# Optimization experiments

Measured on AMD Instinct MI355X. Metric: run time of the kernel, lower is better.

The kernel has to match this reference:

```python
import jax, jax.numpy as jnp
import numpy as np

V, D, H, NB, K = 50257, 768, 128, 4, 4  # vocab, d_model, d_hidden, n_blocks, conv kernel
B, L = 2, 1024


def setup_inputs() -> dict:
    key = jax.random.key(0)
    ks = jax.random.split(key, 8)
    s = 0.02
    return {
        "x": jax.random.randint(ks[0], (B, L), 0, V),
        "embed": jax.random.normal(ks[1], (V, D), jnp.float32) * s,   # tied embedding/head
        "conv_w": jax.random.normal(ks[2], (NB, D, K), jnp.float32) * s,  # depthwise causal conv
        "conv_b": jnp.zeros((NB, D), jnp.float32),
        "W_delta": jax.random.normal(ks[3], (NB, D, H), jnp.float32) * s,
        "b_delta": jnp.zeros((NB, H), jnp.float32),
        "W_in": jax.random.normal(ks[4], (NB, D, H), jnp.float32) * s,
        "W_out": jax.random.normal(ks[5], (NB, H, D), jnp.float32) * s,
        "log_A": jnp.log(jnp.tile(jnp.arange(1, H + 1, dtype=jnp.float32), (NB, 1))),
        "gamma": jnp.ones((D,), jnp.float32),
        "beta": jnp.zeros((D,), jnp.float32),
    }


def _mamba_block(x, cw, cb, Wd, bd, Win, Wout, logA):
    # x: [B,L,D]; cw: [D,K] depthwise causal conv; SSM state size H (shared per example)
    Bsz, Ln, _ = x.shape
    Kk = cw.shape[-1]
    xp = jnp.pad(x, ((0, 0), (Kk - 1, 0), (0, 0)))  # left-pad for causality
    xc = sum(xp[:, j:j + Ln, :] * cw[:, j] for j in range(Kk)) + cb  # [B,L,D]
    u = jax.nn.silu(xc)
    delta = jax.nn.softplus(jnp.einsum('bld,dh->blh', u, Wd) + bd)   # [B,L,H]
    Bu = jnp.einsum('bld,dh->blh', u, Win)                            # [B,L,H]
    A = -jnp.exp(logA)                                                # [H], negative
    decay = jnp.exp(delta * A)   # [B,L,H]
    inc = delta * Bu             # [B,L,H]

    def step(h, t):
        d, z = t
        h = d * h + z
        return h, h

    h0 = jnp.zeros((Bsz, decay.shape[-1]), x.dtype)
    _, hs = jax.lax.scan(step, h0, (decay.transpose(1, 0, 2), inc.transpose(1, 0, 2)))
    hs = hs.transpose(1, 0, 2)                                        # [B,L,H]
    y = jnp.einsum('blh,hd->bld', hs, Wout)
    return x + y  # residual


def reference(x, embed, conv_w, conv_b, W_delta, b_delta, W_in, W_out, log_A, gamma, beta):
    h = embed[x]  # [B,L,D]
    for i in range(conv_w.shape[0]):
        h = _mamba_block(h, conv_w[i], conv_b[i], W_delta[i], b_delta[i],
                         W_in[i], W_out[i], log_A[i])
    mu = jnp.mean(h, -1, keepdims=True)
    var = jnp.var(h, -1, keepdims=True)
    hn = (h - mu) * jax.lax.rsqrt(var + 1e-5) * gamma + beta  # LayerNorm
    return jnp.einsum('bld,vd->blv', hn, embed)  # tied-weight head -> [B,L,V]
```

## Files before the change

kernel.cpp:

```cpp
#include <hip/hip_runtime.h>

#define VSZ   50257
#define VPAD  50304
#define D_    768
#define H_    128
#define BL_   2048
#define LSEQ  1024

typedef __bf16 bf16x8 __attribute__((ext_vector_type(8)));
typedef float  f32x4  __attribute__((ext_vector_type(4)));

__device__ __forceinline__ unsigned short f32_to_bf16(float f) {
  unsigned int u = __float_as_uint(f);
  u += 0x7fffu + ((u >> 16) & 1u);
  return (unsigned short)(u >> 16);
}

__device__ __forceinline__ void gload_lds16(const void* g, void* l) {
  __builtin_amdgcn_global_load_lds((const __attribute__((address_space(1))) void*)g,
                                   (__attribute__((address_space(3))) void*)l,
                                   16, 0, 0);
}

__global__ __launch_bounds__(256) void convert_embed(const float* __restrict__ embed,
                                                     unsigned short* __restrict__ Eb) {
  int idx = blockIdx.x * 256 + threadIdx.x;
  int row = idx / 192;
  ushort4 o;
  if (row < VSZ) {
    float4 f = ((const float4*)embed)[idx];
    o.x = f32_to_bf16(f.x); o.y = f32_to_bf16(f.y);
    o.z = f32_to_bf16(f.z); o.w = f32_to_bf16(f.w);
  } else {
    o = make_ushort4(0, 0, 0, 0);
  }
  ((ushort4*)Eb)[idx] = o;
}

__global__ __launch_bounds__(256) void gather_embed(const int* __restrict__ x,
                                                    const float* __restrict__ embed,
                                                    float* __restrict__ h) {
  int idx = blockIdx.x * 256 + threadIdx.x;
  int m = idx / 192, d4 = idx - m * 192;
  int tok = x[m];
  ((float4*)h)[idx] = ((const float4*)embed)[(size_t)tok * 192 + d4];
}

__global__ __launch_bounds__(256) void conv_silu(const float* __restrict__ h,
                                                 const float* __restrict__ cw,
                                                 const float* __restrict__ cb,
                                                 float* __restrict__ u) {
  int idx = blockIdx.x * 256 + threadIdx.x;
  int m = idx / 192, d4 = idx - m * 192;
  int b = m >> 10, l = m & 1023;
  const float4* cw4 = (const float4*)cw;
  float4 w0 = cw4[d4 * 4 + 0], w1 = cw4[d4 * 4 + 1];
  float4 w2 = cw4[d4 * 4 + 2], w3 = cw4[d4 * 4 + 3];
  float4 acc = ((const float4*)cb)[d4];
  #pragma unroll
  for (int j = 0; j < 4; ++j) {
    int lj = l + j - 3;
    if (lj >= 0) {
      float4 xv = ((const float4*)h)[(size_t)((b << 10) + lj) * 192 + d4];
      acc.x += xv.x * (&w0.x)[j];
      acc.y += xv.y * (&w1.x)[j];
      acc.z += xv.z * (&w2.x)[j];
      acc.w += xv.w * (&w3.x)[j];
    }
  }
  acc.x = acc.x / (1.f + expf(-acc.x));
  acc.y = acc.y / (1.f + expf(-acc.y));
  acc.z = acc.z / (1.f + expf(-acc.z));
  acc.w = acc.w / (1.f + expf(-acc.w));
  ((float4*)u)[idx] = acc;
}

__global__ __launch_bounds__(256) void gemm_dbu(const float* __restrict__ u,
                                                const float* __restrict__ Wd,
                                                const float* __restrict__ Wi,
                                                float* __restrict__ pre) {
  __shared__ float Au[16 * 33];
  int m0 = blockIdx.x * 16;
  int sel = blockIdx.y;
  const float* W = sel ? Wi : Wd;
  int tid = threadIdx.x;
  int tm = tid & 7, tn = tid >> 3;
  float acc[2][4] = {};
  for (int k0 = 0; k0 < 768; k0 += 32) {
    __syncthreads();
    {
      int e = tid;        int mr = e >> 5, k = e & 31;
      Au[mr * 33 + k] = u[(size_t)(m0 + mr) * 768 + k0 + k];
      e = tid + 256;      mr = e >> 5;     k = e & 31;
      Au[mr * 33 + k] = u[(size_t)(m0 + mr) * 768 + k0 + k];
    }
    __syncthreads();
    #pragma unroll 8
    for (int k = 0; k < 32; ++k) {
      float4 w = *(const float4*)&W[(size_t)(k0 + k) * 128 + tn * 4];
      float a0 = Au[(tm * 2 + 0) * 33 + k];
      float a1 = Au[(tm * 2 + 1) * 33 + k];
      acc[0][0] += a0 * w.x; acc[0][1] += a0 * w.y; acc[0][2] += a0 * w.z; acc[0][3] += a0 * w.w;
      acc[1][0] += a1 * w.x; acc[1][1] += a1 * w.y; acc[1][2] += a1 * w.z; acc[1][3] += a1 * w.w;
    }
  }
  #pragma unroll
  for (int mi = 0; mi < 2; ++mi) {
    float4 o = make_float4(acc[mi][0], acc[mi][1], acc[mi][2], acc[mi][3]);
    *(float4*)&pre[(size_t)(m0 + tm * 2 + mi) * 256 + sel * 128 + tn * 4] = o;
  }
}

__device__ __forceinline__ void dz_at(const float* __restrict__ pre, float bdv, float negA,
                                      int m, int hh, float& d, float& z) {
  float pd = pre[(size_t)m * 256 + hh];
  float bu = pre[(size_t)m * 256 + 128 + hh];
  float xx = pd + bdv;
  float delta = (xx > 20.f) ? xx : log1pf(expf(xx));
  d = expf(delta * negA);
  z = delta * bu;
}

__global__ __launch_bounds__(256) void scan_chunks(const float* __restrict__ pre,
                                                   const float* __restrict__ bd,
                                                   const float* __restrict__ logA,
                                                   float* __restrict__ cP,
                                                   float* __restrict__ cQ) {
  int t = blockIdx.x * 256 + threadIdx.x;
  int hh = t & 127, b = (t >> 7) & 1, c = t >> 8;
  float bdv = bd[hh];
  float negA = -expf(logA[hh]);
  float P = 1.f, Q = 0.f;
  int mbase = b * LSEQ + c * 32;
  for (int s = 0; s < 32; ++s) {
    float d, z;
    dz_at(pre, bdv, negA, mbase + s, hh, d, z);
    Q = d * Q + z;
    P *= d;
  }
  int bh = b * 128 + hh;
  cP[c * 256 + bh] = P;
  cQ[c * 256 + bh] = Q;
}

__global__ __launch_bounds__(256) void scan_tops(const float* __restrict__ cP,
                                                 const float* __restrict__ cQ,
                                                 float* __restrict__ sst) {
  int bh = threadIdx.x;
  float s = 0.f;
  for (int c = 0; c < 32; ++c) {
    sst[c * 256 + bh] = s;
    s = cP[c * 256 + bh] * s + cQ[c * 256 + bh];
  }
}

__global__ __launch_bounds__(256) void scan_final(const float* __restrict__ pre,
                                                  const float* __restrict__ bd,
                                                  const float* __restrict__ logA,
                                                  const float* __restrict__ sst,
                                                  float* __restrict__ hsout) {
  int t = blockIdx.x * 256 + threadIdx.x;
  int hh = t & 127, b = (t >> 7) & 1, c = t >> 8;
  float bdv = bd[hh];
  float negA = -expf(logA[hh]);
  int bh = b * 128 + hh;
  float s = sst[c * 256 + bh];
  int mbase = b * LSEQ + c * 32;
  for (int st = 0; st < 32; ++st) {
    float d, z;
    dz_at(pre, bdv, negA, mbase + st, hh, d, z);
    s = d * s + z;
    hsout[(size_t)(mbase + st) * 128 + hh] = s;
  }
}

__global__ __launch_bounds__(256) void gemm_out(const float* __restrict__ hs,
                                                const float* __restrict__ Wout,
                                                float* __restrict__ h) {
  __shared__ float Hs[16 * 129];
  int m0 = blockIdx.x * 16;
  int n0 = blockIdx.y * 128;
  int tid = threadIdx.x;
  int tm = tid & 7, tn = tid >> 3;
  for (int e = tid; e < 2048; e += 256) {
    int mr = e >> 7, k = e & 127;
    Hs[mr * 129 + k] = hs[(size_t)(m0 + mr) * 128 + k];
  }
  __syncthreads();
  float acc[2][4] = {};
  #pragma unroll 4
  for (int k = 0; k < 128; ++k) {
    float4 w = *(const float4*)&Wout[(size_t)k * 768 + n0 + tn * 4];
    float a0 = Hs[(tm * 2 + 0) * 129 + k];
    float a1 = Hs[(tm * 2 + 1) * 129 + k];
    acc[0][0] += a0 * w.x; acc[0][1] += a0 * w.y; acc[0][2] += a0 * w.z; acc[0][3] += a0 * w.w;
    acc[1][0] += a1 * w.x; acc[1][1] += a1 * w.y; acc[1][2] += a1 * w.z; acc[1][3] += a1 * w.w;
  }
  #pragma unroll
  for (int mi = 0; mi < 2; ++mi) {
    size_t o = (size_t)(m0 + tm * 2 + mi) * 768 + n0 + tn * 4;
    float4 r = *(float4*)&h[o];
    r.x += acc[mi][0]; r.y += acc[mi][1]; r.z += acc[mi][2]; r.w += acc[mi][3];
    *(float4*)&h[o] = r;
  }
}

__global__ __launch_bounds__(256) void ln_bf16(const float* __restrict__ h,
                                               const float* __restrict__ gamma,
                                               const float* __restrict__ beta,
                                               unsigned short* __restrict__ hnb) {
  __shared__ float red[10];
  int m = blockIdx.x;
  const float* row = h + (size_t)m * 768;
  int tid = threadIdx.x;
  float a0 = row[tid], a1 = row[tid + 256], a2 = row[tid + 512];
  float s = a0 + a1 + a2;
  float s2 = a0 * a0 + a1 * a1 + a2 * a2;
  #pragma unroll
  for (int o = 32; o > 0; o >>= 1) { s += __shfl_down(s, o); s2 += __shfl_down(s2, o); }
  int wv = tid >> 6;
  if ((tid & 63) == 0) { red[wv] = s; red[4 + wv] = s2; }
  __syncthreads();
  if (tid == 0) {
    float S = red[0] + red[1] + red[2] + red[3];
    float S2 = red[4] + red[5] + red[6] + red[7];
    float mu = S * (1.f / 768.f);
    float var = S2 * (1.f / 768.f) - mu * mu;
    red[8] = mu;
    red[9] = rsqrtf(var + 1e-5f);
  }
  __syncthreads();
  float mu = red[8], rs = red[9];
  unsigned short* orow = hnb + (size_t)m * 768;
  orow[tid]       = f32_to_bf16((a0 - mu) * rs * gamma[tid]       + beta[tid]);
  orow[tid + 256] = f32_to_bf16((a1 - mu) * rs * gamma[tid + 256] + beta[tid + 256]);
  orow[tid + 512] = f32_to_bf16((a2 - mu) * rs * gamma[tid + 512] + beta[tid + 512]);
}

__global__ __launch_bounds__(256) void gemm_head(const unsigned short* __restrict__ Hnb,
                                                 const unsigned short* __restrict__ Eb,
                                                 float* __restrict__ out) {
  __shared__ unsigned short As[128 * 64];
  __shared__ unsigned short Bs[128 * 64];
  const int m0 = blockIdx.x * 128;
  const int v0 = blockIdx.y * 128;
  const int tid = threadIdx.x;
  const int lane = tid & 63;
  const int wave = tid >> 6;
  const int wm = (wave & 1) * 64;
  const int wn = (wave >> 1) * 64;
  const int lrow = lane >> 3;
  const int lcol = (lane & 7) * 8;

  f32x4 acc[4][4];
  #pragma unroll
  for (int i = 0; i < 4; ++i)
    #pragma unroll
    for (int j = 0; j < 4; ++j)
      acc[i][j] = f32x4{0.f, 0.f, 0.f, 0.f};

  for (int k0 = 0; k0 < 768; k0 += 64) {
    #pragma unroll
    for (int inst = 0; inst < 4; ++inst) {
      int c = wave * 4 + inst;
      int r = c * 8 + lrow;
      gload_lds16(Hnb + (size_t)(m0 + r) * 768 + k0 + lcol, &As[c * 512]);
      gload_lds16(Eb  + (size_t)(v0 + r) * 768 + k0 + lcol, &Bs[c * 512]);
    }
    __syncthreads();
    #pragma unroll
    for (int kk = 0; kk < 64; kk += 32) {
      bf16x8 af[4], bfr[4];
      int row_a = wm + (lane & 15);
      int row_b = wn + (lane & 15);
      int coloff = ((lane >> 4) * 8) + kk;
      #pragma unroll
      for (int i = 0; i < 4; ++i)
        af[i] = *(const bf16x8*)(&As[(row_a + i * 16) * 64 + coloff]);
      #pragma unroll
      for (int j = 0; j < 4; ++j)
        bfr[j] = *(const bf16x8*)(&Bs[(row_b + j * 16) * 64 + coloff]);
      #pragma unroll
      for (int i = 0; i < 4; ++i)
        #pragma unroll
        for (int j = 0; j < 4; ++j)
          acc[i][j] = __builtin_amdgcn_mfma_f32_16x16x32_bf16(af[i], bfr[j], acc[i][j], 0, 0, 0);
    }
    __syncthreads();
  }

  const int cr = (lane >> 4) * 4;
  const int cc = lane & 15;
  #pragma unroll
  for (int i = 0; i < 4; ++i) {
    #pragma unroll
    for (int j = 0; j < 4; ++j) {
      int gc = v0 + wn + j * 16 + cc;
      if (gc < VSZ) {
        size_t base = (size_t)(m0 + wm + i * 16 + cr) * VSZ + gc;
        #pragma unroll
        for (int r = 0; r < 4; ++r)
          out[base + (size_t)r * VSZ] = acc[i][j][r];
      }
    }
  }
}

extern "C" void kernel_launch(void* const* d_in, const int* in_sizes, int n_in,
                              void* d_out, int out_size, void* d_ws, size_t ws_size,
                              hipStream_t stream) {
  (void)in_sizes; (void)n_in; (void)out_size; (void)ws_size;
  const int*   x       = (const int*)d_in[0];
  const float* embed   = (const float*)d_in[1];
  const float* conv_w  = (const float*)d_in[2];
  const float* conv_b  = (const float*)d_in[3];
  const float* W_delta = (const float*)d_in[4];
  const float* b_delta = (const float*)d_in[5];
  const float* W_in    = (const float*)d_in[6];
  const float* W_out   = (const float*)d_in[7];
  const float* log_A   = (const float*)d_in[8];
  const float* gamma   = (const float*)d_in[9];
  const float* beta    = (const float*)d_in[10];
  float* out = (float*)d_out;

  char* wsp = (char*)d_ws;
  size_t off = 0;
  auto carve = [&](size_t bytes) -> char* {
    char* p = wsp + off;
    off += (bytes + 255) & ~(size_t)255;
    return p;
  };
  unsigned short* Eb  = (unsigned short*)carve((size_t)VPAD * 768 * 2);
  float* h            = (float*)carve((size_t)BL_ * 768 * 4);
  float* u            = (float*)carve((size_t)BL_ * 768 * 4);
  float* pre          = (float*)carve((size_t)BL_ * 256 * 4);
  float* hsbuf        = (float*)carve((size_t)BL_ * 128 * 4);
  float* cP           = (float*)carve(32 * 256 * 4);
  float* cQ           = (float*)carve(32 * 256 * 4);
  float* sst          = (float*)carve(32 * 256 * 4);
  unsigned short* hnb = (unsigned short*)carve((size_t)BL_ * 768 * 2);

  convert_embed<<<(VPAD * 192) / 256, 256, 0, stream>>>(embed, Eb);
  gather_embed<<<(BL_ * 192) / 256, 256, 0, stream>>>(x, embed, h);

  for (int i = 0; i < 4; ++i) {
    conv_silu<<<(BL_ * 192) / 256, 256, 0, stream>>>(h, conv_w + (size_t)i * 768 * 4,
                                                     conv_b + (size_t)i * 768, u);
    gemm_dbu<<<dim3(128, 2), 256, 0, stream>>>(u, W_delta + (size_t)i * 768 * 128,
                                               W_in + (size_t)i * 768 * 128, pre);
    scan_chunks<<<32, 256, 0, stream>>>(pre, b_delta + i * 128, log_A + i * 128, cP, cQ);
    scan_tops<<<1, 256, 0, stream>>>(cP, cQ, sst);
    scan_final<<<32, 256, 0, stream>>>(pre, b_delta + i * 128, log_A + i * 128, sst, hsbuf);
    gemm_out<<<dim3(128, 6), 256, 0, stream>>>(hsbuf, W_out + (size_t)i * 128 * 768, h);
  }

  ln_bf16<<<BL_, 256, 0, stream>>>(h, gamma, beta, hnb);
  gemm_head<<<dim3(16, 393), 256, 0, stream>>>(hnb, Eb, out);
}
```

Before: 1.324 ms.

## Move block GEMMs to bf16 MFMA, fuse the scan, and swizzle LDS

The scalar fp32 gemm_dbu and gemm_out kernels become a templated bf16 MFMA GEMM that reads pre-transposed bf16 weights, and conv_silu now writes bf16 activations. The three scan kernels merge into one 1024-thread kernel that combines chunk prefixes in shared memory, which cuts launches per block. The head GEMM reuses the same template with an XOR-swizzled LDS layout and nontemporal output stores. Block-path precision drops from fp32 to bf16 inputs, and the scan runs on far fewer workgroups.

```diff
diff --git a/kernel.cpp b/kernel.cpp
--- a/kernel.cpp
+++ b/kernel.cpp
@@ -2,8 +2,6 @@
 
 #define VSZ   50257
 #define VPAD  50304
-#define D_    768
-#define H_    128
 #define BL_   2048
 #define LSEQ  1024
 
@@ -37,6 +35,21 @@
   ((ushort4*)Eb)[idx] = o;
 }
 
+__global__ __launch_bounds__(256) void make_wcat(const float* __restrict__ Wd,
+                                                 const float* __restrict__ Wi,
+                                                 unsigned short* __restrict__ out) {
+  int idx = blockIdx.x * 256 + threadIdx.x;
+  int k = idx % 768, n = (idx / 768) & 255, l = idx / (768 * 256);
+  const float* W = (n < 128) ? Wd : Wi;
+  out[idx] = f32_to_bf16(W[((size_t)l * 768 + k) * 128 + (n & 127)]);
+}
+__global__ __launch_bounds__(256) void make_wout(const float* __restrict__ Wo,
+                                                 unsigned short* __restrict__ out) {
+  int idx = blockIdx.x * 256 + threadIdx.x;
+  int h = idx & 127, d = (idx >> 7) % 768, l = idx / (128 * 768);
+  out[idx] = f32_to_bf16(Wo[((size_t)l * 128 + h) * 768 + d]);
+}
+
 __global__ __launch_bounds__(256) void gather_embed(const int* __restrict__ x,
                                                     const float* __restrict__ embed,
                                                     float* __restrict__ h) {
@@ -49,7 +62,7 @@
 __global__ __launch_bounds__(256) void conv_silu(const float* __restrict__ h,
                                                  const float* __restrict__ cw,
                                                  const float* __restrict__ cb,
-                                                 float* __restrict__ u) {
+                                                 unsigned short* __restrict__ u) {
   int idx = blockIdx.x * 256 + threadIdx.x;
   int m = idx / 192, d4 = idx - m * 192;
   int b = m >> 10, l = m & 1023;
@@ -72,42 +85,84 @@
   acc.y = acc.y / (1.f + expf(-acc.y));
   acc.z = acc.z / (1.f + expf(-acc.z));
   acc.w = acc.w / (1.f + expf(-acc.w));
-  ((float4*)u)[idx] = acc;
-}
-
-__global__ __launch_bounds__(256) void gemm_dbu(const float* __restrict__ u,
-                                                const float* __restrict__ Wd,
-                                                const float* __restrict__ Wi,
-                                                float* __restrict__ pre) {
-  __shared__ float Au[16 * 33];
-  int m0 = blockIdx.x * 16;
-  int sel = blockIdx.y;
-  const float* W = sel ? Wi : Wd;
-  int tid = threadIdx.x;
-  int tm = tid & 7, tn = tid >> 3;
-  float acc[2][4] = {};
-  for (int k0 = 0; k0 < 768; k0 += 32) {
+  ushort4 o;
+  o.x = f32_to_bf16(acc.x); o.y = f32_to_bf16(acc.y);
+  o.z = f32_to_bf16(acc.z); o.w = f32_to_bf16(acc.w);
+  ((ushort4*)u)[idx] = o;
+}
+
+template<int KTOT, int MODE>
+__global__ __launch_bounds__(256) void gemm_mfma(const unsigned short* __restrict__ A,
+                                                 const unsigned short* __restrict__ Bm,
+                                                 float* __restrict__ C, int ldc) {
+  __shared__ unsigned short As[128 * 64];
+  __shared__ unsigned short Bs[128 * 64];
+  const int m0 = blockIdx.x * 128;
+  const int n0 = blockIdx.y * 128;
+  const int tid = threadIdx.x;
+  const int lane = tid & 63;
+  const int wave = tid >> 6;
+  const int wm = (wave & 1) * 64;
+  const int wn = (wave >> 1) * 64;
+  const int lrow = lane >> 3;
+  const int lcol = ((lane & 7) ^ lrow) * 8;
+
+  f32x4 acc[4][4];
+  #pragma unroll
+  for (int i = 0; i < 4; ++i)
+    #pragma unroll
+    for (int j = 0; j < 4; ++j)
+      acc[i][j] = f32x4{0.f, 0.f, 0.f, 0.f};
+
+  for (int k0 = 0; k0 < KTOT; k0 += 64) {
+    #pragma unroll
+    for (int inst = 0; inst < 4; ++inst) {
+      int c = wave * 4 + inst;
+      int r = c * 8 + lrow;
+      gload_lds16(A  + (size_t)(m0 + r) * KTOT + k0 + lcol, &As[c * 512]);
+      gload_lds16(Bm + (size_t)(n0 + r) * KTOT + k0 + lcol, &Bs[c * 512]);
+    }
     __syncthreads();
-    {
-      int e = tid;        int mr = e >> 5, k = e & 31;
-      Au[mr * 33 + k] = u[(size_t)(m0 + mr) * 768 + k0 + k];
-      e = tid + 256;      mr = e >> 5;     k = e & 31;
-      Au[mr * 33 + k] = u[(size_t)(m0 + mr) * 768 + k0 + k];
+    #pragma unroll
+    for (int kk = 0; kk < 64; kk += 32) {
+      bf16x8 af[4], bfr[4];
+      const int frow = lane & 15;
+      const int quad = lane >> 4;
+      const int fx = lane & 7;
+      const int cb = quad + (kk >> 3);
+      const int physc = (cb ^ fx) * 8;
+      #pragma unroll
+      for (int i = 0; i < 4; ++i)
+        af[i] = *(const bf16x8*)(&As[(wm + frow + i * 16) * 64 + physc]);
+      #pragma unroll
+      for (int j = 0; j < 4; ++j)
+        bfr[j] = *(const bf16x8*)(&Bs[(wn + frow + j * 16) * 64 + physc]);
+      #pragma unroll
+      for (int i = 0; i < 4; ++i)
+        #pragma unroll
+        for (int j = 0; j < 4; ++j)
+          acc[i][j] = __builtin_amdgcn_mfma_f32_16x16x32_bf16(af[i], bfr[j], acc[i][j], 0, 0, 0);
     }
     __syncthreads();
-    #pragma unroll 8
-    for (int k = 0; k < 32; ++k) {
-      float4 w = *(const float4*)&W[(size_t)(k0 + k) * 128 + tn * 4];
-      float a0 = Au[(tm * 2 + 0) * 33 + k];
-      float a1 = Au[(tm * 2 + 1) * 33 + k];
-      acc[0][0] += a0 * w.x; acc[0][1] += a0 * w.y; acc[0][2] += a0 * w.z; acc[0][3] += a0 * w.w;
-      acc[1][0] += a1 * w.x; acc[1][1] += a1 * w.y; acc[1][2] += a1 * w.z; acc[1][3] += a1 * w.w;
-    }
-  }
+  }
+
+  const int cr = (lane >> 4) * 4;
+  const int cc = lane & 15;
   #pragma unroll
-  for (int mi = 0; mi < 2; ++mi) {
-    float4 o = make_float4(acc[mi][0], acc[mi][1], acc[mi][2], acc[mi][3]);
-    *(float4*)&pre[(size_t)(m0 + tm * 2 + mi) * 256 + sel * 128 + tn * 4] = o;
+  for (int i = 0; i < 4; ++i) {
+    #pragma unroll
+    for (int j = 0; j < 4; ++j) {
+      int gc = n0 + wn + j * 16 + cc;
+      if (MODE == 2 && gc >= VSZ) continue;
+      size_t base = (size_t)(m0 + wm + i * 16 + cr) * ldc + gc;
+      #pragma unroll
+      for (int r = 0; r < 4; ++r) {
+        float v = acc[i][j][r];
+        if (MODE == 0)      C[base + (size_t)r * ldc] = v;
+        else if (MODE == 1) C[base + (size_t)r * ldc] += v;
+        else                __builtin_nontemporal_store(v, &C[base + (size_t)r * ldc]);
+      }
+    }
   }
 }
 
@@ -121,87 +176,43 @@
   z = delta * bu;
 }
 
-__global__ __launch_bounds__(256) void scan_chunks(const float* __restrict__ pre,
+__global__ __launch_bounds__(1024) void scan_fused(const float* __restrict__ pre,
                                                    const float* __restrict__ bd,
                                                    const float* __restrict__ logA,
-                                                   float* __restrict__ cP,
-                                                   float* __restrict__ cQ) {
-  int t = blockIdx.x * 256 + threadIdx.x;
-  int hh = t & 127, b = (t >> 7) & 1, c = t >> 8;
-  float bdv = bd[hh];
-  float negA = -expf(logA[hh]);
+                                                   unsigned short* __restrict__ hsb) {
+  __shared__ float sP[16][64], sQ[16][64], sS[16][64];
+  const int hl = threadIdx.x & 63;
+  const int c  = threadIdx.x >> 6;
+  const int b  = blockIdx.x;
+  const int hh = blockIdx.y * 64 + hl;
+  const float bdv = bd[hh];
+  const float negA = -expf(logA[hh]);
+  const int mbase = b * LSEQ + c * 64;
+
   float P = 1.f, Q = 0.f;
-  int mbase = b * LSEQ + c * 32;
-  for (int s = 0; s < 32; ++s) {
+  for (int s = 0; s < 64; ++s) {
     float d, z;
     dz_at(pre, bdv, negA, mbase + s, hh, d, z);
     Q = d * Q + z;
     P *= d;
   }
-  int bh = b * 128 + hh;
-  cP[c * 256 + bh] = P;
-  cQ[c * 256 + bh] = Q;
-}
-
-__global__ __launch_bounds__(256) void scan_tops(const float* __restrict__ cP,
-                                                 const float* __restrict__ cQ,
-                                                 float* __restrict__ sst) {
-  int bh = threadIdx.x;
-  float s = 0.f;
-  for (int c = 0; c < 32; ++c) {
-    sst[c * 256 + bh] = s;
-    s = cP[c * 256 + bh] * s + cQ[c * 256 + bh];
-  }
-}
-
-__global__ __launch_bounds__(256) void scan_final(const float* __restrict__ pre,
-                                                  const float* __restrict__ bd,
-                                                  const float* __restrict__ logA,
-                                                  const float* __restrict__ sst,
-                                                  float* __restrict__ hsout) {
-  int t = blockIdx.x * 256 + threadIdx.x;
-  int hh = t & 127, b = (t >> 7) & 1, c = t >> 8;
-  float bdv = bd[hh];
-  float negA = -expf(logA[hh]);
-  int bh = b * 128 + hh;
-  float s = sst[c * 256 + bh];
-  int mbase = b * LSEQ + c * 32;
-  for (int st = 0; st < 32; ++st) {
+  sP[c][hl] = P; sQ[c][hl] = Q;
+  __syncthreads();
+  if (c == 0) {
+    float s = 0.f;
+    #pragma unroll
+    for (int cc2 = 0; cc2 < 16; ++cc2) {
+      sS[cc2][hl] = s;
+      s = sP[cc2][hl] * s + sQ[cc2][hl];
+    }
+  }
+  __syncthreads();
+  float s = sS[c][hl];
+  for (int st = 0; st < 64; ++st) {
     float d, z;
     dz_at(pre, bdv, negA, mbase + st, hh, d, z);
     s = d * s + z;
-    hsout[(size_t)(mbase + st) * 128 + hh] = s;
-  }
-}
-
-__global__ __launch_bounds__(256) void gemm_out(const float* __restrict__ hs,
-                                                const float* __restrict__ Wout,
-                                                float* __restrict__ h) {
-  __shared__ float Hs[16 * 129];
-  int m0 = blockIdx.x * 16;
-  int n0 = blockIdx.y * 128;
-  int tid = threadIdx.x;
-  int tm = tid & 7, tn = tid >> 3;
-  for (int e = tid; e < 2048; e += 256) {
-    int mr = e >> 7, k = e & 127;
-    Hs[mr * 129 + k] = hs[(size_t)(m0 + mr) * 128 + k];
-  }
-  __syncthreads();
-  float acc[2][4] = {};
-  #pragma unroll 4
-  for (int k = 0; k < 128; ++k) {
-    float4 w = *(const float4*)&Wout[(size_t)k * 768 + n0 + tn * 4];
-    float a0 = Hs[(tm * 2 + 0) * 129 + k];
-    float a1 = Hs[(tm * 2 + 1) * 129 + k];
-    acc[0][0] += a0 * w.x; acc[0][1] += a0 * w.y; acc[0][2] += a0 * w.z; acc[0][3] += a0 * w.w;
-    acc[1][0] += a1 * w.x; acc[1][1] += a1 * w.y; acc[1][2] += a1 * w.z; acc[1][3] += a1 * w.w;
-  }
-  #pragma unroll
-  for (int mi = 0; mi < 2; ++mi) {
-    size_t o = (size_t)(m0 + tm * 2 + mi) * 768 + n0 + tn * 4;
-    float4 r = *(float4*)&h[o];
-    r.x += acc[mi][0]; r.y += acc[mi][1]; r.z += acc[mi][2]; r.w += acc[mi][3];
-    *(float4*)&h[o] = r;
+    hsb[(size_t)(mbase + st) * 128 + hh] = f32_to_bf16(s);
   }
 }
 
@@ -237,75 +248,6 @@
   orow[tid + 512] = f32_to_bf16((a2 - mu) * rs * gamma[tid + 512] + beta[tid + 512]);
 }
 
-__global__ __launch_bounds__(256) void gemm_head(const unsigned short* __restrict__ Hnb,
-                                                 const unsigned short* __restrict__ Eb,
-                                                 float* __restrict__ out) {
-  __shared__ unsigned short As[128 * 64];
-  __shared__ unsigned short Bs[128 * 64];
-  const int m0 = blockIdx.x * 128;
-  const int v0 = blockIdx.y * 128;
-  const int tid = threadIdx.x;
-  const int lane = tid & 63;
-  const int wave = tid >> 6;
-  const int wm = (wave & 1) * 64;
-  const int wn = (wave >> 1) * 64;
-  const int lrow = lane >> 3;
-  const int lcol = (lane & 7) * 8;
-
-  f32x4 acc[4][4];
-  #pragma unroll
-  for (int i = 0; i < 4; ++i)
-    #pragma unroll
-    for (int j = 0; j < 4; ++j)
-      acc[i][j] = f32x4{0.f, 0.f, 0.f, 0.f};
-
-  for (int k0 = 0; k0 < 768; k0 += 64) {
-    #pragma unroll
-    for (int inst = 0; inst < 4; ++inst) {
-      int c = wave * 4 + inst;
-      int r = c * 8 + lrow;
-      gload_lds16(Hnb + (size_t)(m0 + r) * 768 + k0 + lcol, &As[c * 512]);
-      gload_lds16(Eb  + (size_t)(v0 + r) * 768 + k0 + lcol, &Bs[c * 512]);
-    }
-    __syncthreads();
-    #pragma unroll
-    for (int kk = 0; kk < 64; kk += 32) {
-      bf16x8 af[4], bfr[4];
-      int row_a = wm + (lane & 15);
-      int row_b = wn + (lane & 15);
-      int coloff = ((lane >> 4) * 8) + kk;
-      #pragma unroll
-      for (int i = 0; i < 4; ++i)
-        af[i] = *(const bf16x8*)(&As[(row_a + i * 16) * 64 + coloff]);
-      #pragma unroll
-      for (int j = 0; j < 4; ++j)
-        bfr[j] = *(const bf16x8*)(&Bs[(row_b + j * 16) * 64 + coloff]);
-      #pragma unroll
-      for (int i = 0; i < 4; ++i)
-        #pragma unroll
-        for (int j = 0; j < 4; ++j)
-          acc[i][j] = __builtin_amdgcn_mfma_f32_16x16x32_bf16(af[i], bfr[j], acc[i][j], 0, 0, 0);
-    }
-    __syncthreads();
-  }
-
-  const int cr = (lane >> 4) * 4;
-  const int cc = lane & 15;
-  #pragma unroll
-  for (int i = 0; i < 4; ++i) {
-    #pragma unroll
-    for (int j = 0; j < 4; ++j) {
-      int gc = v0 + wn + j * 16 + cc;
-      if (gc < VSZ) {
-        size_t base = (size_t)(m0 + wm + i * 16 + cr) * VSZ + gc;
-        #pragma unroll
-        for (int r = 0; r < 4; ++r)
-          out[base + (size_t)r * VSZ] = acc[i][j][r];
-      }
-    }
-  }
-}
-
 extern "C" void kernel_launch(void* const* d_in, const int* in_sizes, int n_in,
                               void* d_out, int out_size, void* d_ws, size_t ws_size,
                               hipStream_t stream) {
@@ -330,30 +272,30 @@
     off += (bytes + 255) & ~(size_t)255;
     return p;
   };
-  unsigned short* Eb  = (unsigned short*)carve((size_t)VPAD * 768 * 2);
-  float* h            = (float*)carve((size_t)BL_ * 768 * 4);
-  float* u            = (float*)carve((size_t)BL_ * 768 * 4);
-  float* pre          = (float*)carve((size_t)BL_ * 256 * 4);
-  float* hsbuf        = (float*)carve((size_t)BL_ * 128 * 4);
-  float* cP           = (float*)carve(32 * 256 * 4);
-  float* cQ           = (float*)carve(32 * 256 * 4);
-  float* sst          = (float*)carve(32 * 256 * 4);
-  unsigned short* hnb = (unsigned short*)carve((size_t)BL_ * 768 * 2);
+  unsigned short* Eb    = (unsigned short*)carve((size_t)VPAD * 768 * 2);
+  unsigned short* WcatT = (unsigned short*)carve((size_t)4 * 256 * 768 * 2);
+  unsigned short* WoutT = (unsigned short*)carve((size_t)4 * 768 * 128 * 2);
+  float*          h     = (float*)carve((size_t)BL_ * 768 * 4);
+  unsigned short* u     = (unsigned short*)carve((size_t)BL_ * 768 * 2);
+  float*          pre   = (float*)carve((size_t)BL_ * 256 * 4);
+  unsigned short* hs    = (unsigned short*)carve((size_t)BL_ * 128 * 2);
+  unsigned short* hnb   = (unsigned short*)carve((size_t)BL_ * 768 * 2);
 
   convert_embed<<<(VPAD * 192) / 256, 256, 0, stream>>>(embed, Eb);
+  make_wcat<<<(4 * 256 * 768) / 256, 256, 0, stream>>>(W_delta, W_in, WcatT);
+  make_wout<<<(4 * 768 * 128) / 256, 256, 0, stream>>>(W_out, WoutT);
   gather_embed<<<(BL_ * 192) / 256, 256, 0, stream>>>(x, embed, h);
 
   for (int i = 0; i < 4; ++i) {
     conv_silu<<<(BL_ * 192) / 256, 256, 0, stream>>>(h, conv_w + (size_t)i * 768 * 4,
                                                      conv_b + (size_t)i * 768, u);
-    gemm_dbu<<<dim3(128, 2), 256, 0, stream>>>(u, W_delta + (size_t)i * 768 * 128,
-                                               W_in + (size_t)i * 768 * 128, pre);
-    scan_chunks<<<32, 256, 0, stream>>>(pre, b_delta + i * 128, log_A + i * 128, cP, cQ);
-    scan_tops<<<1, 256, 0, stream>>>(cP, cQ, sst);
-    scan_final<<<32, 256, 0, stream>>>(pre, b_delta + i * 128, log_A + i * 128, sst, hsbuf);
-    gemm_out<<<dim3(128, 6), 256, 0, stream>>>(hsbuf, W_out + (size_t)i * 128 * 768, h);
+    gemm_mfma<768, 0><<<dim3(16, 2), 256, 0, stream>>>(u, WcatT + (size_t)i * 256 * 768,
+                                                       pre, 256);
+    scan_fused<<<dim3(2, 2), 1024, 0, stream>>>(pre, b_delta + i * 128, log_A + i * 128, hs);
+    gemm_mfma<128, 1><<<dim3(16, 6), 256, 0, stream>>>(hs, WoutT + (size_t)i * 768 * 128,
+                                                       h, 768);
   }
 
   ln_bf16<<<BL_, 256, 0, stream>>>(h, gamma, beta, hnb);
-  gemm_head<<<dim3(16, 393), 256, 0, stream>>>(hnb, Eb, out);
-}
+  gemm_mfma<768, 2><<<dim3(16, 393), 256, 0, stream>>>(hnb, Eb, out, VSZ);
+}
```

Result: slower. 1.538 ms (+16.2%).
